# Kernel optimization log

Hardware: AMD Instinct MI355X
Metric: run time of the kernel (lower is better)

The kernel has to match this reference:

```python
import jax, jax.numpy as jnp
import numpy as np

B, H, W, R, C = 4, 64, 64, 64, 32  # batch, height, width, in-channels r, conv out-channels


def setup_inputs() -> dict:
    key = jax.random.key(0)
    kx, kf, kg = jax.random.split(key, 3)
    x = jax.random.normal(kx, (B, H, W, R), dtype=jnp.float32)
    # 1x1 conv with in_channels=1: kernel is effectively a length-C vector
    w_f = jax.random.normal(kf, (C,), dtype=jnp.float32) * 0.1
    w_g = jax.random.normal(kg, (C,), dtype=jnp.float32) * 0.1
    gamma = jnp.ones((), dtype=jnp.float32)
    return {"x": x, "w_f": w_f, "w_g": w_g, "gamma": gamma}


def reference(x, w_f, w_g, gamma):
    b, h, w, r = x.shape
    hw = h * w
    xs = x.reshape(b, hw, r)                      # [B, HW, R]
    # conv_f / conv_g: each scalar of xs times weight vector -> [B, HW, R*C]
    x_f = (xs[..., None] * w_f).reshape(b, hw, -1)
    x_g = (xs[..., None] * w_g).reshape(b, hw, -1)
    attn = jnp.einsum('bik,bjk->bij', x_f, x_g)   # [B, HW, HW]
    attn = jax.nn.softmax(attn, axis=-1) * gamma
    # out[b,j,r] = sum_i attn[b,j,i] * xs[b,i,r]
    out = jnp.einsum('bji,bir->bjr', attn, xs)
    return out.reshape(b, h, w, r)
```

## Files before the change

### kernel.cpp

```cpp
#include <hip/hip_runtime.h>


#define N_SEQ 4096
#define KS    4
#define LOG2E 1.4426950408889634f

typedef __attribute__((ext_vector_type(8))) short short8;
typedef __attribute__((ext_vector_type(4))) short short4v;
typedef __attribute__((ext_vector_type(4))) float f4;

union U8 { short8 v8; short4v v4[2]; unsigned short u[8]; };

#define MFMA16(a,b,c) __builtin_amdgcn_mfma_f32_16x16x32_bf16(a,b,c,0,0,0)

static __device__ __forceinline__ unsigned short f2bf(float f){
  unsigned int u = __float_as_uint(f);
  u += 0x7fffu + ((u>>16)&1u);
  return (unsigned short)(u>>16);
}
static __device__ __forceinline__ float bf2f(unsigned short b){
  return __uint_as_float(((unsigned int)b)<<16);
}
static __device__ __forceinline__ float fexp2(float x){
#if __has_builtin(__builtin_amdgcn_exp2f)
  return __builtin_amdgcn_exp2f(x);
#else
  return exp2f(x);
#endif
}
static __device__ __forceinline__ f4 splat4(float v){ f4 r; r.x=v; r.y=v; r.z=v; r.w=v; return r; }
static __device__ __forceinline__ f4 exp2v(f4 v){
  f4 r; r.x=fexp2(v.x); r.y=fexp2(v.y); r.z=fexp2(v.z); r.w=fexp2(v.w); return r;
}
static __device__ __forceinline__ f4 max4(f4 a, f4 b){
  f4 r; r.x=fmaxf(a.x,b.x); r.y=fmaxf(a.y,b.y); r.z=fmaxf(a.z,b.z); r.w=fmaxf(a.w,b.w); return r;
}
static __device__ __forceinline__ f4 shx4(f4 v, int m){
  f4 r; r.x=__shfl_xor(v.x,m,64); r.y=__shfl_xor(v.y,m,64);
        r.z=__shfl_xor(v.z,m,64); r.w=__shfl_xor(v.w,m,64); return r;
}
static __device__ __forceinline__ void gld_lds16(const void* g, void* l){
  __builtin_amdgcn_global_load_lds(
      (const __attribute__((address_space(1))) unsigned int*)g,
      (__attribute__((address_space(3))) unsigned int*)l, 16, 0, 0);
}

__global__ __launch_bounds__(256) void prep_kernel(
    const float* __restrict__ x, unsigned short* __restrict__ xhi,
    unsigned short* __restrict__ xt)
{
  __shared__ unsigned short T[64][66];
  const int tid = threadIdx.x;
  const int bb  = blockIdx.x >> 6;
  const int n0  = (blockIdx.x & 63) << 6;
  {
    const int r  = tid >> 2;
    const int c4 = tid & 3;
    const float* src = x + ((size_t)(bb*N_SEQ + n0 + r))*64 + c4*16;
    unsigned short h[16];
    #pragma unroll
    for (int i = 0; i < 4; ++i) {
      const float4 f = *(const float4*)(src + i*4);
      h[i*4+0]=f2bf(f.x); h[i*4+1]=f2bf(f.y); h[i*4+2]=f2bf(f.z); h[i*4+3]=f2bf(f.w);
    }
    unsigned short* dst = xhi + ((size_t)(bb*N_SEQ + n0 + r))*64 + c4*16;
    U8 u0, u1;
    #pragma unroll
    for (int j = 0; j < 8; ++j) { u0.u[j]=h[j]; u1.u[j]=h[8+j]; }
    *(short8*)dst = u0.v8; *(short8*)(dst+8) = u1.v8;
    #pragma unroll
    for (int j = 0; j < 16; ++j) T[r][c4*16+j] = h[j];
  }
  __syncthreads();
  {
    const int d = tid >> 2;
    const int g = tid & 3;
    unsigned short o[16];
    #pragma unroll
    for (int j = 0; j < 16; ++j) o[j] = T[g*16+j][d];
    unsigned short* dst = xt + ((size_t)(bb*64 + d))*N_SEQ + n0 + g*16;
    U8 u0, u1;
    #pragma unroll
    for (int j = 0; j < 8; ++j) { u0.u[j]=o[j]; u1.u[j]=o[8+j]; }
    *(short8*)dst = u0.v8; *(short8*)(dst+8) = u1.v8;
  }
}

#define LDP 36

__global__ __launch_bounds__(256, 3) void fattn_split_kernel(
    const float* __restrict__ x, const float* __restrict__ wf,
    const float* __restrict__ wg,
    const unsigned short* __restrict__ xhi, const unsigned short* __restrict__ xt,
    float* __restrict__ OP, float* __restrict__ LP)
{
  __shared__ __align__(16) unsigned short KHI[2][4096];
  __shared__ __align__(16) unsigned short VT [2][4096];
  __shared__ __align__(16) unsigned short PB [4][32*LDP];

  const int tid  = threadIdx.x;
  const int lane = tid & 63;
  const int wv   = tid >> 6;
  const int mg   = wv & 1;
  const int hh   = wv >> 1;
  const int quad = lane >> 4;
  const int l15  = lane & 15;
  const int swz  = l15 & 7;
  const int ks   = blockIdx.x >> 8;
  const int rem  = blockIdx.x & 255;
  const int bb   = rem >> 6;
  const int qb   = (rem & 63) << 6;

  float s = 0.f;
  #pragma unroll
  for (int i = 0; i < 32; ++i) s += wf[i]*wg[i];
  const float s2 = s * LOG2E;

  const float* xb = x + ((size_t)bb * N_SEQ) * 64;

  short8 qhf[2][2], qlf[2][2];
  #pragma unroll
  for (int mt = 0; mt < 2; ++mt) {
    const int row = qb + mg*32 + mt*16 + l15;
    #pragma unroll
    for (int c = 0; c < 2; ++c) {
      const float* src = xb + row*64 + c*32 + quad*8;
      const float4 a0 = *(const float4*)src;
      const float4 a1 = *(const float4*)(src+4);
      float qv[8] = {a0.x,a0.y,a0.z,a0.w,a1.x,a1.y,a1.z,a1.w};
      U8 vh, vl;
      #pragma unroll
      for (int j = 0; j < 8; ++j) {
        float q = qv[j]*s2;
        unsigned short hb = f2bf(q);
        vh.u[j] = (short)hb;
        vl.u[j] = (short)f2bf(q - bf2f(hb));
      }
      qhf[mt][c] = vh.v8; qlf[mt][c] = vl.v8;
    }
  }

  f4 Oc[2][4], ls[2];
  #pragma unroll
  for (int mt = 0; mt < 2; ++mt) {
    ls[mt] = splat4(0.f);
    #pragma unroll
    for (int nt = 0; nt < 4; ++nt) Oc[mt][nt] = splat4(0.f);
  }

  const int kbb = ks*1024;

  #pragma unroll 1
  for (int t = 0; t < 8; ++t) {
    const int kt = kbb + t*64;
    #pragma unroll
    for (int i = 0; i < 8; ++i) {
      const int reg = i >> 1;
      const int h   = reg & 1;
      const int ch  = wv*2 + (i & 1);
      const int p   = ch*64 + lane;
      const int rr  = p >> 3;
      const int cg  = (p & 7) ^ (rr & 7);
      if (reg < 2) {
        const unsigned short* g = xhi + ((size_t)(bb*N_SEQ + kt + h*512 + rr))*64 + cg*8;
        gld_lds16(g, &KHI[h][ch*512]);
      } else {
        const unsigned short* g = xt + ((size_t)(bb*64 + rr))*N_SEQ + (kt + h*512 + cg*8);
        gld_lds16(g, &VT[h][ch*512]);
      }
    }
    __syncthreads();

    f4 Sa[2][4];
    #pragma unroll
    for (int mt = 0; mt < 2; ++mt)
      #pragma unroll
      for (int n = 0; n < 4; ++n) Sa[mt][n] = splat4(0.f);

    #pragma unroll
    for (int n = 0; n < 4; ++n) {
      #pragma unroll
      for (int c = 0; c < 2; ++c) {
        const int idx = (n*16 + l15)*64 + ((c*4 + quad) ^ swz)*8;
        const short8 bh = *(const short8*)&KHI[hh][idx];
        #pragma unroll
        for (int mt = 0; mt < 2; ++mt) {
          Sa[mt][n] = MFMA16(qhf[mt][c], bh, Sa[mt][n]);
          Sa[mt][n] = MFMA16(qlf[mt][c], bh, Sa[mt][n]);
        }
      }
    }

    f4 p[2][4];
    #pragma unroll
    for (int mt = 0; mt < 2; ++mt) {
      #pragma unroll
      for (int n = 0; n < 4; ++n) { p[mt][n] = exp2v(Sa[mt][n]); ls[mt] += p[mt][n]; }
    }

    #pragma unroll
    for (int kc = 0; kc < 2; ++kc) {
      #pragma unroll
      for (int mt = 0; mt < 2; ++mt) {
        #pragma unroll
        for (int n2 = 0; n2 < 2; ++n2) {
          const f4 pv = p[mt][kc*2+n2];
          const int base = (mt*16 + quad*4)*LDP + n2*16 + l15;
          PB[wv][base        ] = f2bf(pv.x);
          PB[wv][base +   LDP] = f2bf(pv.y);
          PB[wv][base + 2*LDP] = f2bf(pv.z);
          PB[wv][base + 3*LDP] = f2bf(pv.w);
        }
      }
      short8 pa[2];
      #pragma unroll
      for (int mt = 0; mt < 2; ++mt) {
        U8 u;
        const int rb = (mt*16 + l15)*LDP + quad*8;
        u.v4[0] = *(const short4v*)&PB[wv][rb];
        u.v4[1] = *(const short4v*)&PB[wv][rb+4];
        pa[mt] = u.v8;
      }
      #pragma unroll
      for (int nt = 0; nt < 4; ++nt) {
        const int idxv = (nt*16 + l15)*64 + ((kc*4 + quad) ^ swz)*8;
        const short8 vb = *(const short8*)&VT[hh][idxv];
        #pragma unroll
        for (int mt = 0; mt < 2; ++mt) Oc[mt][nt] = MFMA16(pa[mt], vb, Oc[mt][nt]);
      }
    }
    __syncthreads();
  }

  #pragma unroll
  for (int mt = 0; mt < 2; ++mt) {
    ls[mt] += shx4(ls[mt],1); ls[mt] += shx4(ls[mt],2);
    ls[mt] += shx4(ls[mt],4); ls[mt] += shx4(ls[mt],8);
  }

  float* MO = (float*)KHI;
  float* ML = (float*)VT;
  if (hh == 1) {
    #pragma unroll
    for (int mt = 0; mt < 2; ++mt) {
      const int rbase = mg*32 + mt*16 + quad*4;
      #pragma unroll
      for (int nt = 0; nt < 4; ++nt) {
        MO[(rbase+0)*64 + nt*16 + l15] = Oc[mt][nt].x;
        MO[(rbase+1)*64 + nt*16 + l15] = Oc[mt][nt].y;
        MO[(rbase+2)*64 + nt*16 + l15] = Oc[mt][nt].z;
        MO[(rbase+3)*64 + nt*16 + l15] = Oc[mt][nt].w;
      }
      if (l15 == 0) {
        ML[rbase+0] = ls[mt].x; ML[rbase+1] = ls[mt].y;
        ML[rbase+2] = ls[mt].z; ML[rbase+3] = ls[mt].w;
      }
    }
  }
  __syncthreads();
  if (hh == 0) {
    float* op = OP + (size_t)blockIdx.x * 4096;
    #pragma unroll
    for (int mt = 0; mt < 2; ++mt) {
      const int rbase = mg*32 + mt*16 + quad*4;
      #pragma unroll
      for (int nt = 0; nt < 4; ++nt) {
        #pragma unroll
        for (int rg = 0; rg < 4; ++rg) {
          const int rr = rbase + rg;
          op[rr*64 + nt*16 + l15] = Oc[mt][nt][rg] + MO[rr*64 + nt*16 + l15];
        }
      }
      if (l15 == 0) {
        #pragma unroll
        for (int rg = 0; rg < 4; ++rg)
          LP[(size_t)blockIdx.x*64 + rbase + rg] = ls[mt][rg] + ML[rbase+rg];
      }
    }
  }
}

__global__ __launch_bounds__(256) void merge_kernel(
    const float* __restrict__ OP, const float* __restrict__ LP,
    const float* __restrict__ gm, float* __restrict__ out)
{
  const int idx = blockIdx.x*256 + threadIdx.x;
  const int e0  = idx*4;
  const int d0  = e0 & 63;
  const int row = e0 >> 6;
  const int bb  = row >> 12;
  const int q   = row & 4095;
  const int qt  = q >> 6;
  const int qr  = q & 63;
  float4 acc = make_float4(0.f,0.f,0.f,0.f);
  float l = 0.f;
  #pragma unroll
  for (int sct = 0; sct < KS; ++sct) {
    const int blk = sct*256 + bb*64 + qt;
    const float4 o = *(const float4*)(OP + (size_t)blk*4096 + qr*64 + d0);
    acc.x += o.x; acc.y += o.y; acc.z += o.z; acc.w += o.w;
    l += LP[(size_t)blk*64 + qr];
  }
  const float w = gm[0] / l;
  float4 r; r.x = acc.x*w; r.y = acc.y*w; r.z = acc.z*w; r.w = acc.w*w;
  *(float4*)(out + e0) = r;
}

#define LDKF 72
#define TILEF (64*LDKF)

__global__ __launch_bounds__(256) void fattn_fallback(
    const float* __restrict__ x, const float* __restrict__ wf,
    const float* __restrict__ wg, const float* __restrict__ gm,
    float* __restrict__ out)
{
  __shared__ __align__(16) unsigned short KHI[2*TILEF];
  __shared__ __align__(16) unsigned short KLO[2*TILEF];
  __shared__ __align__(16) unsigned short VT [2*TILEF];
  __shared__ __align__(16) unsigned short PB [4*32*LDP];

  const int tid  = threadIdx.x;
  const int lane = tid & 63;
  const int wv   = tid >> 6;
  const int mg   = wv & 1;
  const int hh   = wv >> 1;
  const int quad = lane >> 4;
  const int l15  = lane & 15;
  const int bb   = blockIdx.x >> 6;
  const int qb   = (blockIdx.x & 63) << 6;

  float s = 0.f;
  #pragma unroll
  for (int i = 0; i < 32; ++i) s += wf[i]*wg[i];
  const float s2 = s * LOG2E;
  const float gamma = gm[0];

  const float* xb = x + ((size_t)bb * N_SEQ) * 64;

  short8 qhf[2][2], qlf[2][2];
  #pragma unroll
  for (int mt = 0; mt < 2; ++mt) {
    const int row = qb + mg*32 + mt*16 + l15;
    #pragma unroll
    for (int c = 0; c < 2; ++c) {
      const float* src = xb + row*64 + c*32 + quad*8;
      const float4 a0 = *(const float4*)src;
      const float4 a1 = *(const float4*)(src+4);
      float qv[8] = {a0.x,a0.y,a0.z,a0.w,a1.x,a1.y,a1.z,a1.w};
      U8 vh, vl;
      #pragma unroll
      for (int j = 0; j < 8; ++j) {
        float q = qv[j]*s2;
        unsigned short hb = f2bf(q);
        vh.u[j] = (short)hb;
        vl.u[j] = (short)f2bf(q - bf2f(hb));
      }
      qhf[mt][c] = vh.v8; qlf[mt][c] = vl.v8;
    }
  }

  f4 Oc[2][4], mo[2], ls[2];
  #pragma unroll
  for (int mt = 0; mt < 2; ++mt) {
    mo[mt] = splat4(-1e30f);
    ls[mt] = splat4(0.f);
    #pragma unroll
    for (int nt = 0; nt < 4; ++nt) Oc[mt][nt] = splat4(0.f);
  }

  const int sh   = tid >> 7;
  const int srow = (tid & 127) >> 1;
  const int sch  = tid & 1;

  float4 sr[8];
  {
    const float* sp = xb + (sh*2048 + srow)*64 + sch*32;
    #pragma unroll
    for (int i = 0; i < 8; ++i) sr[i] = *(const float4*)(sp + i*4);
    unsigned short hb[32], lb[32];
    #pragma unroll
    for (int i = 0; i < 8; ++i) {
      float vv[4] = {sr[i].x, sr[i].y, sr[i].z, sr[i].w};
      #pragma unroll
      for (int j = 0; j < 4; ++j) {
        unsigned short h = f2bf(vv[j]);
        hb[i*4+j] = h;
        lb[i*4+j] = f2bf(vv[j] - bf2f(h));
      }
    }
    const int kbase = sh*TILEF + srow*LDKF + sch*32;
    #pragma unroll
    for (int g = 0; g < 4; ++g) {
      U8 wh, wl;
      #pragma unroll
      for (int j = 0; j < 8; ++j) { wh.u[j]=(short)hb[g*8+j]; wl.u[j]=(short)lb[g*8+j]; }
      *(short8*)&KHI[kbase+g*8] = wh.v8;
      *(short8*)&KLO[kbase+g*8] = wl.v8;
    }
    #pragma unroll
    for (int j = 0; j < 32; ++j) VT[sh*TILEF + (sch*32+j)*LDKF + srow] = hb[j];
  }
  __syncthreads();

  #pragma unroll 1
  for (int t = 0; t < 32; ++t) {
    if (t+1 < 32) {
      const float* sp = xb + (sh*2048 + (t+1)*64 + srow)*64 + sch*32;
      #pragma unroll
      for (int i = 0; i < 8; ++i) sr[i] = *(const float4*)(sp + i*4);
    }

    f4 Sa[2][4];
    #pragma unroll
    for (int mt = 0; mt < 2; ++mt)
      #pragma unroll
      for (int n = 0; n < 4; ++n) Sa[mt][n] = splat4(0.f);

    const int kldsb = hh*TILEF;
    #pragma unroll
    for (int n = 0; n < 4; ++n) {
      #pragma unroll
      for (int c = 0; c < 2; ++c) {
        const int off = kldsb + (n*16 + l15)*LDKF + c*32 + quad*8;
        const short8 bh = *(const short8*)&KHI[off];
        const short8 bl = *(const short8*)&KLO[off];
        #pragma unroll
        for (int mt = 0; mt < 2; ++mt) {
          Sa[mt][n] = MFMA16(qhf[mt][c], bh, Sa[mt][n]);
          Sa[mt][n] = MFMA16(qlf[mt][c], bh, Sa[mt][n]);
          Sa[mt][n] = MFMA16(qhf[mt][c], bl, Sa[mt][n]);
        }
      }
    }

    f4 p[2][4];
    #pragma unroll
    for (int mt = 0; mt < 2; ++mt) {
      f4 rm = max4(max4(Sa[mt][0],Sa[mt][1]), max4(Sa[mt][2],Sa[mt][3]));
      rm = max4(rm, shx4(rm,1));
      rm = max4(rm, shx4(rm,2));
      rm = max4(rm, shx4(rm,4));
      rm = max4(rm, shx4(rm,8));
      f4 mn = max4(mo[mt], rm);
      f4 al = exp2v(mo[mt] - mn);
      mo[mt] = mn;
      f4 rs = splat4(0.f);
      #pragma unroll
      for (int n = 0; n < 4; ++n) { p[mt][n] = exp2v(Sa[mt][n] - mn); rs += p[mt][n]; }
      rs += shx4(rs,1); rs += shx4(rs,2); rs += shx4(rs,4); rs += shx4(rs,8);
      ls[mt] = ls[mt]*al + rs;
      #pragma unroll
      for (int nt = 0; nt < 4; ++nt) Oc[mt][nt] *= al;
    }

    const int pw = wv * (32*LDP);
    #pragma unroll
    for (int kc = 0; kc < 2; ++kc) {
      #pragma unroll
      for (int mt = 0; mt < 2; ++mt) {
        #pragma unroll
        for (int n2 = 0; n2 < 2; ++n2) {
          const f4 pv = p[mt][kc*2+n2];
          const int base = pw + (mt*16 + quad*4)*LDP + n2*16 + l15;
          ((unsigned short*)PB)[base        ] = f2bf(pv.x);
          ((unsigned short*)PB)[base +   LDP] = f2bf(pv.y);
          ((unsigned short*)PB)[base + 2*LDP] = f2bf(pv.z);
          ((unsigned short*)PB)[base + 3*LDP] = f2bf(pv.w);
        }
      }
      short8 pa[2];
      #pragma unroll
      for (int mt = 0; mt < 2; ++mt) {
        U8 u;
        const int rb = pw + (mt*16 + l15)*LDP + quad*8;
        u.v4[0] = *(const short4v*)&((unsigned short*)PB)[rb];
        u.v4[1] = *(const short4v*)&((unsigned short*)PB)[rb+4];
        pa[mt] = u.v8;
      }
      #pragma unroll
      for (int nt = 0; nt < 4; ++nt) {
        const short8 vb = *(const short8*)&VT[kldsb + (nt*16 + l15)*LDKF + kc*32 + quad*8];
        #pragma unroll
        for (int mt = 0; mt < 2; ++mt) Oc[mt][nt] = MFMA16(pa[mt], vb, Oc[mt][nt]);
      }
    }

    __syncthreads();

    if (t+1 < 32) {
      unsigned short hb[32], lb[32];
      #pragma unroll
      for (int i = 0; i < 8; ++i) {
        float vv[4] = {sr[i].x, sr[i].y, sr[i].z, sr[i].w};
        #pragma unroll
        for (int j = 0; j < 4; ++j) {
          unsigned short h = f2bf(vv[j]);
          hb[i*4+j] = h;
          lb[i*4+j] = f2bf(vv[j] - bf2f(h));
        }
      }
      const int kbase = sh*TILEF + srow*LDKF + sch*32;
      #pragma unroll
      for (int g = 0; g < 4; ++g) {
        U8 wh, wl;
        #pragma unroll
        for (int j = 0; j < 8; ++j) { wh.u[j]=(short)hb[g*8+j]; wl.u[j]=(short)lb[g*8+j]; }
        *(short8*)&KHI[kbase+g*8] = wh.v8;
        *(short8*)&KLO[kbase+g*8] = wl.v8;
      }
      #pragma unroll
      for (int j = 0; j < 32; ++j) VT[sh*TILEF + (sch*32+j)*LDKF + srow] = hb[j];
      __syncthreads();
    }
  }

  float* MO  = (float*)KHI;
  float* MML = (float*)KLO;
  if (hh == 1) {
    #pragma unroll
    for (int mt = 0; mt < 2; ++mt) {
      const int rbase = mg*32 + mt*16 + quad*4;
      #pragma unroll
      for (int nt = 0; nt < 4; ++nt) {
        MO[(rbase+0)*64 + nt*16 + l15] = Oc[mt][nt].x;
        MO[(rbase+1)*64 + nt*16 + l15] = Oc[mt][nt].y;
        MO[(rbase+2)*64 + nt*16 + l15] = Oc[mt][nt].z;
        MO[(rbase+3)*64 + nt*16 + l15] = Oc[mt][nt].w;
      }
      if (l15 == 0) {
        MML[rbase+0] = mo[mt].x; MML[rbase+1] = mo[mt].y;
        MML[rbase+2] = mo[mt].z; MML[rbase+3] = mo[mt].w;
        MML[64+rbase+0] = ls[mt].x; MML[64+rbase+1] = ls[mt].y;
        MML[64+rbase+2] = ls[mt].z; MML[64+rbase+3] = ls[mt].w;
      }
    }
  }
  __syncthreads();
  if (hh == 0) {
    #pragma unroll
    for (int mt = 0; mt < 2; ++mt) {
      const int rbase = mg*32 + mt*16 + quad*4;
      f4 m1, l1;
      m1.x = MML[rbase+0]; m1.y = MML[rbase+1]; m1.z = MML[rbase+2]; m1.w = MML[rbase+3];
      l1.x = MML[64+rbase+0]; l1.y = MML[64+rbase+1]; l1.z = MML[64+rbase+2]; l1.w = MML[64+rbase+3];
      const f4 mn = max4(mo[mt], m1);
      const f4 a0 = exp2v(mo[mt] - mn);
      const f4 a1 = exp2v(m1 - mn);
      f4 lt = ls[mt]*a0 + l1*a1;
      f4 w; w.x = gamma/lt.x; w.y = gamma/lt.y; w.z = gamma/lt.z; w.w = gamma/lt.w;
      #pragma unroll
      for (int nt = 0; nt < 4; ++nt) {
        #pragma unroll
        for (int rg = 0; rg < 4; ++rg) {
          const int rr = rbase + rg;
          const float o1 = MO[rr*64 + nt*16 + l15];
          const float val = (Oc[mt][nt][rg]*a0[rg] + o1*a1[rg]) * w[rg];
          out[((size_t)bb*N_SEQ + qb + rr)*64 + nt*16 + l15] = val;
        }
      }
    }
  }
}

extern "C" void kernel_launch(void* const* d_in, const int* in_sizes, int n_in,
                              void* d_out, int out_size, void* d_ws, size_t ws_size,
                              hipStream_t stream) {
  const float* x  = (const float*)d_in[0];
  const float* wf = (const float*)d_in[1];
  const float* wg = (const float*)d_in[2];
  const float* gm = (const float*)d_in[3];
  float* out = (float*)d_out;

  const size_t XHI_OFF = 0;
  const size_t XT_OFF  = 2097152;
  const size_t OP_OFF  = 4194304;
  const size_t LP_OFF  = 20971520;
  const size_t NEED    = 21233664;

  if (ws_size >= NEED) {
    unsigned short* xhi = (unsigned short*)((char*)d_ws + XHI_OFF);
    unsigned short* xt  = (unsigned short*)((char*)d_ws + XT_OFF);
    float* OP = (float*)((char*)d_ws + OP_OFF);
    float* LP = (float*)((char*)d_ws + LP_OFF);
    prep_kernel<<<dim3(256), dim3(256), 0, stream>>>(x, xhi, xt);
    fattn_split_kernel<<<dim3(KS*256), dim3(256), 0, stream>>>(x, wf, wg, xhi, xt, OP, LP);
    merge_kernel<<<dim3(1024), dim3(256), 0, stream>>>(OP, LP, gm, out);
  } else {
    fattn_fallback<<<dim3(256), dim3(256), 0, stream>>>(x, wf, wg, gm, out);
  }
}
```

Measured before the change: 107.3 us.

## Switch attention MFMAs to fp16 and compute transposed scores to simplify P staging

Converts K, V and P from bf16 to fp16 via packed round-toward-zero conversion and drops the hi/lo split of Q, which halves the QK^T MFMA count. Scores are now computed as K·Q^T, so each lane writes P to LDS as one 4-element vector store and reads it back as one 8-element load instead of scalar transposed stores. Row sums are reduced with two shuffles instead of four. The softmax skips max subtraction, so fp16 with its narrower exponent range and lower accuracy in Q and P could overflow or lose precision relative to the bf16 hi/lo scheme.

```diff
diff --git a/kernel.cpp b/kernel.cpp
--- a/kernel.cpp
+++ b/kernel.cpp
@@ -4,14 +4,23 @@
 #define N_SEQ 4096
 #define KS    4
 #define LOG2E 1.4426950408889634f
+#define LDP2  72
 
 typedef __attribute__((ext_vector_type(8))) short short8;
 typedef __attribute__((ext_vector_type(4))) short short4v;
 typedef __attribute__((ext_vector_type(4))) float f4;
-
-union U8 { short8 v8; short4v v4[2]; unsigned short u[8]; };
+typedef _Float16 half8  __attribute__((ext_vector_type(8)));
+typedef _Float16 half4v __attribute__((ext_vector_type(4)));
+typedef _Float16 half2t __attribute__((ext_vector_type(2)));
+typedef __fp16   fp16x2 __attribute__((ext_vector_type(2)));
+
+union U8  { short8 v8; short4v v4[2]; unsigned short u[8]; };
+union HU8 { half8 v; half2t h2[4]; unsigned short u[8]; };
+union HU4 { half4v v; half2t h2[2]; unsigned short u[4]; };
+union PK  { fp16x2 f; half2t h; };
 
 #define MFMA16(a,b,c) __builtin_amdgcn_mfma_f32_16x16x32_bf16(a,b,c,0,0,0)
+#define MFMAH(a,b,c)  __builtin_amdgcn_mfma_f32_16x16x32_f16(a,b,c,0,0,0)
 
 static __device__ __forceinline__ unsigned short f2bf(float f){
   unsigned int u = __float_as_uint(f);
@@ -20,6 +29,14 @@
 }
 static __device__ __forceinline__ float bf2f(unsigned short b){
   return __uint_as_float(((unsigned int)b)<<16);
+}
+static __device__ __forceinline__ half2t pkrtz(float a, float b){
+#if __has_builtin(__builtin_amdgcn_cvt_pkrtz)
+  PK u; u.f = __builtin_amdgcn_cvt_pkrtz(a, b);
+  return u.h;
+#else
+  half2t r; r.x = (_Float16)a; r.y = (_Float16)b; return r;
+#endif
 }
 static __device__ __forceinline__ float fexp2(float x){
 #if __has_builtin(__builtin_amdgcn_exp2f)
@@ -46,7 +63,7 @@
 }
 
 __global__ __launch_bounds__(256) void prep_kernel(
-    const float* __restrict__ x, unsigned short* __restrict__ xhi,
+    const float* __restrict__ x, unsigned short* __restrict__ xh,
     unsigned short* __restrict__ xt)
 {
   __shared__ unsigned short T[64][66];
@@ -61,9 +78,10 @@
     #pragma unroll
     for (int i = 0; i < 4; ++i) {
       const float4 f = *(const float4*)(src + i*4);
-      h[i*4+0]=f2bf(f.x); h[i*4+1]=f2bf(f.y); h[i*4+2]=f2bf(f.z); h[i*4+3]=f2bf(f.w);
-    }
-    unsigned short* dst = xhi + ((size_t)(bb*N_SEQ + n0 + r))*64 + c4*16;
+      HU4 u; u.h2[0] = pkrtz(f.x, f.y); u.h2[1] = pkrtz(f.z, f.w);
+      h[i*4+0]=u.u[0]; h[i*4+1]=u.u[1]; h[i*4+2]=u.u[2]; h[i*4+3]=u.u[3];
+    }
+    unsigned short* dst = xh + ((size_t)(bb*N_SEQ + n0 + r))*64 + c4*16;
     U8 u0, u1;
     #pragma unroll
     for (int j = 0; j < 8; ++j) { u0.u[j]=h[j]; u1.u[j]=h[8+j]; }
@@ -86,17 +104,15 @@
   }
 }
 
-#define LDP 36
-
-__global__ __launch_bounds__(256, 3) void fattn_split_kernel(
+__global__ __launch_bounds__(256, 3) void fattn2_kernel(
     const float* __restrict__ x, const float* __restrict__ wf,
     const float* __restrict__ wg,
-    const unsigned short* __restrict__ xhi, const unsigned short* __restrict__ xt,
+    const unsigned short* __restrict__ xh, const unsigned short* __restrict__ xt,
     float* __restrict__ OP, float* __restrict__ LP)
 {
-  __shared__ __align__(16) unsigned short KHI[2][4096];
-  __shared__ __align__(16) unsigned short VT [2][4096];
-  __shared__ __align__(16) unsigned short PB [4][32*LDP];
+  __shared__ __align__(16) unsigned short KH[2][4096];
+  __shared__ __align__(16) unsigned short VT[2][4096];
+  __shared__ __align__(16) unsigned short PB[4][32*LDP2];
 
   const int tid  = threadIdx.x;
   const int lane = tid & 63;
@@ -118,7 +134,7 @@
 
   const float* xb = x + ((size_t)bb * N_SEQ) * 64;
 
-  short8 qhf[2][2], qlf[2][2];
+  half8 qf[2][2];
   #pragma unroll
   for (int mt = 0; mt < 2; ++mt) {
     const int row = qb + mg*32 + mt*16 + l15;
@@ -127,28 +143,26 @@
       const float* src = xb + row*64 + c*32 + quad*8;
       const float4 a0 = *(const float4*)src;
       const float4 a1 = *(const float4*)(src+4);
-      float qv[8] = {a0.x,a0.y,a0.z,a0.w,a1.x,a1.y,a1.z,a1.w};
-      U8 vh, vl;
-      #pragma unroll
-      for (int j = 0; j < 8; ++j) {
-        float q = qv[j]*s2;
-        unsigned short hb = f2bf(q);
-        vh.u[j] = (short)hb;
-        vl.u[j] = (short)f2bf(q - bf2f(hb));
-      }
-      qhf[mt][c] = vh.v8; qlf[mt][c] = vl.v8;
-    }
-  }
-
-  f4 Oc[2][4], ls[2];
+      HU8 u;
+      u.h2[0] = pkrtz(a0.x*s2, a0.y*s2);
+      u.h2[1] = pkrtz(a0.z*s2, a0.w*s2);
+      u.h2[2] = pkrtz(a1.x*s2, a1.y*s2);
+      u.h2[3] = pkrtz(a1.z*s2, a1.w*s2);
+      qf[mt][c] = u.v;
+    }
+  }
+
+  f4 Oc[2][4];
+  f4 lsa[2];
   #pragma unroll
   for (int mt = 0; mt < 2; ++mt) {
-    ls[mt] = splat4(0.f);
+    lsa[mt] = splat4(0.f);
     #pragma unroll
     for (int nt = 0; nt < 4; ++nt) Oc[mt][nt] = splat4(0.f);
   }
 
   const int kbb = ks*1024;
+  unsigned short* PBw = PB[wv];
 
   #pragma unroll 1
   for (int t = 0; t < 8; ++t) {
@@ -162,83 +176,70 @@
       const int rr  = p >> 3;
       const int cg  = (p & 7) ^ (rr & 7);
       if (reg < 2) {
-        const unsigned short* g = xhi + ((size_t)(bb*N_SEQ + kt + h*512 + rr))*64 + cg*8;
-        gld_lds16(g, &KHI[h][ch*512]);
+        gld_lds16(xh + ((size_t)(bb*N_SEQ + kt + h*512 + rr))*64 + cg*8, &KH[h][ch*512]);
       } else {
-        const unsigned short* g = xt + ((size_t)(bb*64 + rr))*N_SEQ + (kt + h*512 + cg*8);
-        gld_lds16(g, &VT[h][ch*512]);
+        gld_lds16(xt + ((size_t)(bb*64 + rr))*N_SEQ + (kt + h*512 + cg*8), &VT[h][ch*512]);
       }
     }
     __syncthreads();
 
-    f4 Sa[2][4];
-    #pragma unroll
-    for (int mt = 0; mt < 2; ++mt)
-      #pragma unroll
-      for (int n = 0; n < 4; ++n) Sa[mt][n] = splat4(0.f);
-
-    #pragma unroll
-    for (int n = 0; n < 4; ++n) {
-      #pragma unroll
-      for (int c = 0; c < 2; ++c) {
-        const int idx = (n*16 + l15)*64 + ((c*4 + quad) ^ swz)*8;
-        const short8 bh = *(const short8*)&KHI[hh][idx];
-        #pragma unroll
-        for (int mt = 0; mt < 2; ++mt) {
-          Sa[mt][n] = MFMA16(qhf[mt][c], bh, Sa[mt][n]);
-          Sa[mt][n] = MFMA16(qlf[mt][c], bh, Sa[mt][n]);
-        }
-      }
-    }
-
-    f4 p[2][4];
-    #pragma unroll
-    for (int mt = 0; mt < 2; ++mt) {
-      #pragma unroll
-      for (int n = 0; n < 4; ++n) { p[mt][n] = exp2v(Sa[mt][n]); ls[mt] += p[mt][n]; }
+    f4 St[4][2];
+    #pragma unroll
+    for (int k2 = 0; k2 < 4; ++k2)
+      #pragma unroll
+      for (int mt = 0; mt < 2; ++mt) St[k2][mt] = splat4(0.f);
+
+    #pragma unroll
+    for (int c = 0; c < 2; ++c) {
+      half8 kf[4];
+      #pragma unroll
+      for (int k2 = 0; k2 < 4; ++k2)
+        kf[k2] = *(const half8*)&KH[hh][(k2*16 + l15)*64 + (((c*4 + quad) ^ swz))*8];
+      #pragma unroll
+      for (int k2 = 0; k2 < 4; ++k2)
+        #pragma unroll
+        for (int mt = 0; mt < 2; ++mt)
+          St[k2][mt] = MFMAH(kf[k2], qf[mt][c], St[k2][mt]);
+    }
+
+    #pragma unroll
+    for (int k2 = 0; k2 < 4; ++k2) {
+      #pragma unroll
+      for (int mt = 0; mt < 2; ++mt) {
+        const f4 p = exp2v(St[k2][mt]);
+        lsa[mt] += p;
+        HU4 u; u.h2[0] = pkrtz(p.x, p.y); u.h2[1] = pkrtz(p.z, p.w);
+        *(half4v*)&PBw[(mt*16 + l15)*LDP2 + k2*16 + quad*4] = u.v;
+      }
     }
 
     #pragma unroll
     for (int kc = 0; kc < 2; ++kc) {
-      #pragma unroll
-      for (int mt = 0; mt < 2; ++mt) {
-        #pragma unroll
-        for (int n2 = 0; n2 < 2; ++n2) {
-          const f4 pv = p[mt][kc*2+n2];
-          const int base = (mt*16 + quad*4)*LDP + n2*16 + l15;
-          PB[wv][base        ] = f2bf(pv.x);
-          PB[wv][base +   LDP] = f2bf(pv.y);
-          PB[wv][base + 2*LDP] = f2bf(pv.z);
-          PB[wv][base + 3*LDP] = f2bf(pv.w);
-        }
-      }
-      short8 pa[2];
-      #pragma unroll
-      for (int mt = 0; mt < 2; ++mt) {
-        U8 u;
-        const int rb = (mt*16 + l15)*LDP + quad*8;
-        u.v4[0] = *(const short4v*)&PB[wv][rb];
-        u.v4[1] = *(const short4v*)&PB[wv][rb+4];
-        pa[mt] = u.v8;
-      }
+      half8 pa[2];
+      #pragma unroll
+      for (int mt = 0; mt < 2; ++mt)
+        pa[mt] = *(const half8*)&PBw[(mt*16 + l15)*LDP2 + kc*32 + quad*8];
       #pragma unroll
       for (int nt = 0; nt < 4; ++nt) {
-        const int idxv = (nt*16 + l15)*64 + ((kc*4 + quad) ^ swz)*8;
-        const short8 vb = *(const short8*)&VT[hh][idxv];
-        #pragma unroll
-        for (int mt = 0; mt < 2; ++mt) Oc[mt][nt] = MFMA16(pa[mt], vb, Oc[mt][nt]);
+        const half8 vb = *(const half8*)&VT[hh][(nt*16 + l15)*64 + (((kc*4 + quad) ^ swz))*8];
+        #pragma unroll
+        for (int mt = 0; mt < 2; ++mt)
+          Oc[mt][nt] = MFMAH(pa[mt], vb, Oc[mt][nt]);
       }
     }
     __syncthreads();
   }
 
+  float lsum[2];
   #pragma unroll
   for (int mt = 0; mt < 2; ++mt) {
-    ls[mt] += shx4(ls[mt],1); ls[mt] += shx4(ls[mt],2);
-    ls[mt] += shx4(ls[mt],4); ls[mt] += shx4(ls[mt],8);
-  }
-
-  float* MO = (float*)KHI;
+    float sv = lsa[mt].x + lsa[mt].y + lsa[mt].z + lsa[mt].w;
+    sv += __shfl_xor(sv, 16, 64);
+    sv += __shfl_xor(sv, 32, 64);
+    lsum[mt] = sv;
+  }
+
+  float* MO = (float*)KH;
   float* ML = (float*)VT;
   if (hh == 1) {
     #pragma unroll
@@ -251,10 +252,7 @@
         MO[(rbase+2)*64 + nt*16 + l15] = Oc[mt][nt].z;
         MO[(rbase+3)*64 + nt*16 + l15] = Oc[mt][nt].w;
       }
-      if (l15 == 0) {
-        ML[rbase+0] = ls[mt].x; ML[rbase+1] = ls[mt].y;
-        ML[rbase+2] = ls[mt].z; ML[rbase+3] = ls[mt].w;
-      }
+      if (quad == 0) ML[mg*32 + mt*16 + l15] = lsum[mt];
     }
   }
   __syncthreads();
@@ -271,11 +269,8 @@
           op[rr*64 + nt*16 + l15] = Oc[mt][nt][rg] + MO[rr*64 + nt*16 + l15];
         }
       }
-      if (l15 == 0) {
-        #pragma unroll
-        for (int rg = 0; rg < 4; ++rg)
-          LP[(size_t)blockIdx.x*64 + rbase + rg] = ls[mt][rg] + ML[rbase+rg];
-      }
+      if (quad == 0)
+        LP[(size_t)blockIdx.x*64 + mg*32 + mt*16 + l15] = lsum[mt] + ML[mg*32 + mt*16 + l15];
     }
   }
 }
@@ -308,6 +303,7 @@
 
 #define LDKF 72
 #define TILEF (64*LDKF)
+#define LDP 36
 
 __global__ __launch_bounds__(256) void fattn_fallback(
     const float* __restrict__ x, const float* __restrict__ wf,
@@ -571,19 +567,19 @@
   const float* gm = (const float*)d_in[3];
   float* out = (float*)d_out;
 
-  const size_t XHI_OFF = 0;
-  const size_t XT_OFF  = 2097152;
-  const size_t OP_OFF  = 4194304;
-  const size_t LP_OFF  = 20971520;
-  const size_t NEED    = 21233664;
+  const size_t XH_OFF = 0;
+  const size_t XT_OFF = 2097152;
+  const size_t OP_OFF = 4194304;
+  const size_t LP_OFF = 20971520;
+  const size_t NEED   = 21233664;
 
   if (ws_size >= NEED) {
-    unsigned short* xhi = (unsigned short*)((char*)d_ws + XHI_OFF);
-    unsigned short* xt  = (unsigned short*)((char*)d_ws + XT_OFF);
+    unsigned short* xhp = (unsigned short*)((char*)d_ws + XH_OFF);
+    unsigned short* xtp = (unsigned short*)((char*)d_ws + XT_OFF);
     float* OP = (float*)((char*)d_ws + OP_OFF);
     float* LP = (float*)((char*)d_ws + LP_OFF);
-    prep_kernel<<<dim3(256), dim3(256), 0, stream>>>(x, xhi, xt);
-    fattn_split_kernel<<<dim3(KS*256), dim3(256), 0, stream>>>(x, wf, wg, xhi, xt, OP, LP);
+    prep_kernel<<<dim3(256), dim3(256), 0, stream>>>(x, xhp, xtp);
+    fattn2_kernel<<<dim3(KS*256), dim3(256), 0, stream>>>(x, wf, wg, xhp, xtp, OP, LP);
     merge_kernel<<<dim3(1024), dim3(256), 0, stream>>>(OP, LP, gm, out);
   } else {
     fattn_fallback<<<dim3(256), dim3(256), 0, stream>>>(x, wf, wg, gm, out);
```

Measured after the change: 97.98 us. 8.7% less time.
